# Kernel tuning notes

Measured on AMD Instinct MI355X. Metric: run time of the kernel, lower is better.

The kernel has to match this reference:

```python
import jax, jax.numpy as jnp
import numpy as np

N_NODES = 100000
N_EDGES = 1600000
D = 128


def _graph_conv(x, src, dst, norm_src, norm_dst, W, b):
    # DGL GraphConv, norm='both': out = D_dst^{-1/2} A D_src^{-1/2} x W + b
    xs = x * norm_src[:, None]                 # [N, d] scale by src (out-)degree
    agg = jax.ops.segment_sum(xs[src], dst, num_segments=N_NODES)  # SpMM
    hd = agg * norm_dst[:, None]
    return hd @ W + b


def setup_inputs() -> dict:
    key = jax.random.key(0)
    ks = jax.random.split(key, 9)
    h = jax.random.normal(ks[0], (N_NODES, D), dtype=jnp.float32)
    src = jax.random.randint(ks[1], (N_EDGES,), 0, N_NODES, dtype=jnp.int64)
    dst = jax.random.randint(ks[2], (N_EDGES,), 0, N_NODES, dtype=jnp.int64)
    s = 1.0 / np.sqrt(D)
    W0 = jax.random.uniform(ks[3], (D, D), jnp.float32, -s, s)
    b0 = jnp.zeros((D,), jnp.float32)
    W1 = jax.random.uniform(ks[4], (D, D), jnp.float32, -s, s)
    b1 = jnp.zeros((D,), jnp.float32)
    W2 = jax.random.uniform(ks[5], (D, D), jnp.float32, -s, s)
    b2 = jnp.zeros((D,), jnp.float32)
    return {"h": h, "src": src, "dst": dst, "W0": W0, "b0": b0,
            "W1": W1, "b1": b1, "W2": W2, "b2": b2}


def reference(h, src, dst, W0, b0, W1, b1, W2, b2):
    ones = jnp.ones((N_EDGES,), jnp.float32)
    deg_out = jnp.maximum(jax.ops.segment_sum(ones, src, num_segments=N_NODES), 1.0)
    deg_in = jnp.maximum(jax.ops.segment_sum(ones, dst, num_segments=N_NODES), 1.0)
    norm_src = deg_out ** -0.5
    norm_dst = deg_in ** -0.5

    x = jax.nn.relu(_graph_conv(h, src, dst, norm_src, norm_dst, W0, b0))
    x = jax.nn.relu(_graph_conv(x, src, dst, norm_src, norm_dst, W1, b1))
    x = _graph_conv(x, src, dst, norm_src, norm_dst, W2, b2)
    # dgl.mean_nodes over a single graph -> [1, out_size]
    return jnp.mean(x, axis=0, keepdims=True)
```

## Files before the change

### kernel.cpp

```cpp
#include <hip/hip_runtime.h>
#include <hip/hip_fp16.h>

#define N_NODES 100000
#define N_EDGES 1600000
#define D 128
#define SCAN_NB ((N_NODES + 1023) / 1024)
#define CHK 128
#define CHUNK_E (N_EDGES / CHK)
#define QTR_N 25000
#define QTR_U (QTR_N / 4)
#define PP_STRIDE (N_NODES / 4)
#define NSH8 8
#define SH8 (N_NODES / NSH8)
#define SH8_U (SH8 / 4)

typedef _Float16 f16x4 __attribute__((ext_vector_type(4)));
typedef _Float16 f16x8 __attribute__((ext_vector_type(8)));
typedef float f32x4 __attribute__((ext_vector_type(4)));
typedef float f32x2 __attribute__((ext_vector_type(2)));

__global__ __launch_bounds__(256) void
k_hist(const int* __restrict__ src, const int* __restrict__ dst,
       unsigned int* __restrict__ pp) {
    __shared__ unsigned int h[QTR_U];
    int b = blockIdx.x;
    int arr = b >> 9, q = (b >> 7) & 3, c = b & (CHK - 1);
    const int* a = arr ? dst : src;
    int lo = q * QTR_N;
    for (int i = threadIdx.x; i < QTR_U; i += 256) h[i] = 0;
    __syncthreads();
    int e0 = c * CHUNK_E;
    for (int i = e0 + threadIdx.x; i < e0 + CHUNK_E; i += 256) {
        int v = a[i] - lo;
        if ((unsigned)v < QTR_N)
            atomicAdd(&h[v >> 2], 1u << ((v & 3) * 8));
    }
    __syncthreads();
    unsigned int* po = pp + ((size_t)(arr * CHK + c)) * PP_STRIDE + q * QTR_U;
    for (int i = threadIdx.x; i < QTR_U; i += 256) po[i] = h[i];
}

__global__ void k_merge(unsigned int* __restrict__ pp,
                        int* __restrict__ cnt_src, int* __restrict__ cnt_dst) {
    int g = blockIdx.x * blockDim.x + threadIdx.x;
    if (g >= 2 * PP_STRIDE) return;
    int arr = g / PP_STRIDE, u = g % PP_STRIDE;
    unsigned int* p = pp + ((size_t)arr * CHK) * PP_STRIDE + u;
    int s0 = 0, s1 = 0, s2 = 0, s3 = 0;
#pragma unroll 8
    for (int c = 0; c < CHK; c++) {
        unsigned int v = p[(size_t)c * PP_STRIDE];
        p[(size_t)c * PP_STRIDE] =
            (unsigned)s0 | ((unsigned)s1 << 8) | ((unsigned)s2 << 16) | ((unsigned)s3 << 24);
        s0 += v & 255; s1 += (v >> 8) & 255; s2 += (v >> 16) & 255; s3 += (v >> 24) & 255;
    }
    int* cnt = arr ? cnt_dst : cnt_src;
    cnt[4 * u + 0] = s0; cnt[4 * u + 1] = s1; cnt[4 * u + 2] = s2; cnt[4 * u + 3] = s3;
}

__global__ __launch_bounds__(1024) void
k_scan1(const int* __restrict__ cnt_dst, const int* __restrict__ cnt_src,
        int* __restrict__ rpD, int* __restrict__ rpS,
        int* __restrict__ bsD, int* __restrict__ bsS) {
    __shared__ int s[1024];
    int arr = blockIdx.x / SCAN_NB, bb = blockIdx.x % SCAN_NB;
    const int* cnt = arr ? cnt_src : cnt_dst;
    int* rp1 = (arr ? rpS : rpD) + 1;
    int* bs = arr ? bsS : bsD;
    int tid = threadIdx.x;
    int i = bb * 1024 + tid;
    int v = (i < N_NODES) ? cnt[i] : 0;
    s[tid] = v;
    __syncthreads();
    for (int d = 1; d < 1024; d <<= 1) {
        int t = (tid >= d) ? s[tid - d] : 0;
        __syncthreads();
        s[tid] += t;
        __syncthreads();
    }
    if (i < N_NODES) rp1[i] = s[tid];
    if (tid == 1023) bs[bb] = s[1023];
}

__global__ void k_scan2(int* __restrict__ bsD, int* __restrict__ bsS) {
    __shared__ int s[128];
    int* bs = blockIdx.x ? bsS : bsD;
    int tid = threadIdx.x;
    int v = (tid < SCAN_NB) ? bs[tid] : 0;
    s[tid] = v;
    __syncthreads();
    for (int d = 1; d < 128; d <<= 1) {
        int t = (tid >= d) ? s[tid - d] : 0;
        __syncthreads();
        s[tid] += t;
        __syncthreads();
    }
    if (tid < SCAN_NB) bs[tid] = s[tid] - v;
}

__global__ void k_scan3norm(int* __restrict__ rpD, int* __restrict__ rpS,
                            const int* __restrict__ bsD, const int* __restrict__ bsS,
                            const int* __restrict__ cnt_src, const int* __restrict__ cnt_dst,
                            float* __restrict__ ns, float* __restrict__ nd,
                            float* __restrict__ colsum) {
    int i = blockIdx.x * blockDim.x + threadIdx.x;
    if (i >= N_NODES) return;
    rpD[1 + i] += bsD[i >> 10];
    rpS[1 + i] += bsS[i >> 10];
    if (i == 0) { rpD[0] = 0; rpS[0] = 0; }
    if (i < 128) colsum[i] = 0.0f;
    ns[i] = rsqrtf((float)max(cnt_src[i], 1));
    nd[i] = rsqrtf((float)max(cnt_dst[i], 1));
}

__global__ __launch_bounds__(256) void
k_scatter_both(const int* __restrict__ src, const int* __restrict__ dst,
               const int* __restrict__ rpD, const int* __restrict__ rpS,
               const unsigned int* __restrict__ pp, const float* __restrict__ nd,
               int* __restrict__ csr_src, float* __restrict__ csrv) {
    __shared__ unsigned int cur[SH8_U];
    int which = blockIdx.x >> 10;
    int b = blockIdx.x & 1023;
    int sh = b & 7, c = b >> 3;
    int lo = sh * SH8;
    for (int i = threadIdx.x; i < SH8_U; i += 256) cur[i] = 0;
    __syncthreads();
    int e0 = c * CHUNK_E;
    if (which == 0) {
        const unsigned int* pre = pp + ((size_t)(CHK + c)) * PP_STRIDE;
        for (int i = e0 + threadIdx.x; i < e0 + CHUNK_E; i += 256) {
            int dfull = dst[i];
            int d = dfull - lo;
            if ((unsigned)d < SH8) {
                int sft = (d & 3) * 8;
                int rank = (atomicAdd(&cur[d >> 2], 1u << sft) >> sft) & 255;
                int p8 = (pre[dfull >> 2] >> ((dfull & 3) * 8)) & 255;
                csr_src[rpD[dfull] + p8 + rank] = src[i];
            }
        }
    } else {
        const unsigned int* pre = pp + (size_t)c * PP_STRIDE;
        for (int i = e0 + threadIdx.x; i < e0 + CHUNK_E; i += 256) {
            int sfull = src[i];
            int s = sfull - lo;
            if ((unsigned)s < SH8) {
                int sft = (s & 3) * 8;
                int rank = (atomicAdd(&cur[s >> 2], 1u << sft) >> sft) & 255;
                int p8 = (pre[sfull >> 2] >> ((sfull & 3) * 8)) & 255;
                csrv[rpS[sfull] + p8 + rank] = nd[dst[i]];
            }
        }
    }
}

__global__ void k_wsum(const int* __restrict__ rpS, const float* __restrict__ csrv,
                       const float* __restrict__ ns, float* __restrict__ wsum) {
    int gid = blockIdx.x * blockDim.x + threadIdx.x;
    int wv = gid >> 6, lane = gid & 63;
    int n = wv * 16 + (lane & 15);
    int off = lane >> 4;
    float s = 0.0f;
    int beg = 0, end = 0;
    if (n < N_NODES) { beg = rpS[n]; end = rpS[n + 1]; }
    for (int j = beg + off; j < end; j += 4) s += csrv[j];
    s += __shfl_xor(s, 16, 64);
    s += __shfl_xor(s, 32, 64);
    if (n < N_NODES && lane < 16) wsum[n] = s * ns[n];
}

__global__ void k_prep(const float* __restrict__ W0, const float* __restrict__ W1,
                       __half* __restrict__ Wt, const float* __restrict__ x,
                       const float* __restrict__ ns, unsigned int* __restrict__ out) {
    if (blockIdx.x < 128) {
        int i = blockIdx.x * 256 + threadIdx.x;
        int l = i >> 14, r = i & (D * D - 1);
        int n = r >> 7, k = r & 127;
        const float* W = l ? W1 : W0;
        Wt[i] = __float2half(W[k * D + n]);
        return;
    }
    int i = (blockIdx.x - 128) * 256 + threadIdx.x;
    if (i >= N_NODES * (D / 4)) return;
    int n = i >> 5;
    float4 v = ((const float4*)x)[i];
    float s = ns[n];
    int u = __builtin_amdgcn_cvt_pk_fp8_f32(v.x * s, v.y * s, 0, false);
    u = __builtin_amdgcn_cvt_pk_fp8_f32(v.z * s, v.w * s, u, true);
    out[i] = (unsigned int)u;
}

__global__ __launch_bounds__(256) void
k_spmm(const unsigned char* __restrict__ x8, const int* __restrict__ row_ptr,
       const int* __restrict__ csr_src, __half* __restrict__ agg) {
    int wave = (blockIdx.x * blockDim.x + threadIdx.x) >> 6;
    int lane = threadIdx.x & 63;
    int hf = lane >> 5, l32 = lane & 31;
    if (wave >= N_NODES) return;
    int beg = row_ptr[wave], end = row_ptr[wave + 1];
    float a0 = 0.f, a1 = 0.f, a2 = 0.f, a3 = 0.f;
    int j = beg;
    for (; j + 7 < end; j += 8) {
#pragma unroll
        for (int p = 0; p < 4; p++) {
            int s0 = csr_src[j + 2 * p];
            int s1 = csr_src[j + 2 * p + 1];
            int s = hf ? s1 : s0;
            unsigned int u = *(const unsigned int*)(x8 + (size_t)s * D + 4 * l32);
            f32x2 lo = __builtin_amdgcn_cvt_pk_f32_fp8(u, false);
            f32x2 hi = __builtin_amdgcn_cvt_pk_f32_fp8(u, true);
            a0 += lo[0]; a1 += lo[1]; a2 += hi[0]; a3 += hi[1];
        }
    }
    for (; j + 1 < end; j += 2) {
        int s0 = csr_src[j], s1 = csr_src[j + 1];
        int s = hf ? s1 : s0;
        unsigned int u = *(const unsigned int*)(x8 + (size_t)s * D + 4 * l32);
        f32x2 lo = __builtin_amdgcn_cvt_pk_f32_fp8(u, false);
        f32x2 hi = __builtin_amdgcn_cvt_pk_f32_fp8(u, true);
        a0 += lo[0]; a1 += lo[1]; a2 += hi[0]; a3 += hi[1];
    }
    if (j < end && hf == 0) {
        int s = csr_src[j];
        unsigned int u = *(const unsigned int*)(x8 + (size_t)s * D + 4 * l32);
        f32x2 lo = __builtin_amdgcn_cvt_pk_f32_fp8(u, false);
        f32x2 hi = __builtin_amdgcn_cvt_pk_f32_fp8(u, true);
        a0 += lo[0]; a1 += lo[1]; a2 += hi[0]; a3 += hi[1];
    }
    a0 += __shfl_xor(a0, 32, 64);
    a1 += __shfl_xor(a1, 32, 64);
    a2 += __shfl_xor(a2, 32, 64);
    a3 += __shfl_xor(a3, 32, 64);
    if (hf == 0) {
        f16x4 o;
        o[0] = (_Float16)a0; o[1] = (_Float16)a1; o[2] = (_Float16)a2; o[3] = (_Float16)a3;
        ((f16x4*)(agg + (size_t)wave * D))[l32] = o;
    }
}

__global__ __launch_bounds__(256) void
k_gemm_mfma(const __half* __restrict__ A, const __half* __restrict__ Wt,
            const float* __restrict__ b, const float* __restrict__ nd,
            const float* __restrict__ ns, unsigned char* __restrict__ out) {
    int w = threadIdx.x >> 6, lane = threadIdx.x & 63;
    int m = lane & 15, q = lane >> 4;
    int row0 = blockIdx.x * 128 + w * 32;

    f16x8 zf;
#pragma unroll
    for (int j = 0; j < 8; j++) zf[j] = (_Float16)0;
    f16x8 af[2][4];
#pragma unroll
    for (int g = 0; g < 2; g++) {
        int arow = row0 + g * 16 + m;
        const f16x8* pa = (const f16x8*)(A + (size_t)arow * D);
        bool aok = arow < N_NODES;
#pragma unroll
        for (int ks = 0; ks < 4; ks++) af[g][ks] = aok ? pa[ks * 4 + q] : zf;
    }

    const f16x8* pb = (const f16x8*)Wt;
    f32x4 acc[2][8];
#pragma unroll
    for (int g = 0; g < 2; g++)
#pragma unroll
        for (int nt = 0; nt < 8; nt++) acc[g][nt] = (f32x4){0.f, 0.f, 0.f, 0.f};

#pragma unroll
    for (int ks = 0; ks < 4; ks++) {
#pragma unroll
        for (int nt = 0; nt < 8; nt++) {
            f16x8 bf = pb[((nt * 16 + m) << 4) + (ks << 2) + q];
            acc[0][nt] = __builtin_amdgcn_mfma_f32_16x16x32_f16(af[0][ks], bf, acc[0][nt], 0, 0, 0);
            acc[1][nt] = __builtin_amdgcn_mfma_f32_16x16x32_f16(af[1][ks], bf, acc[1][nt], 0, 0, 0);
        }
    }

#pragma unroll
    for (int g = 0; g < 2; g++) {
        int er = row0 + g * 16 + q * 4;
        float sd[4], ss[4];
#pragma unroll
        for (int r = 0; r < 4; r++) {
            int n = er + r;
            bool ok = n < N_NODES;
            sd[r] = ok ? nd[n] : 0.0f;
            ss[r] = ok ? ns[n] : 0.0f;
        }
#pragma unroll
        for (int nt = 0; nt < 8; nt++) {
            int col = nt * 16 + m;
            float bc = b[col];
#pragma unroll
            for (int r = 0; r < 4; r++) {
                int n = er + r;
                if (n < N_NODES) {
                    float v = fmaxf(sd[r] * acc[g][nt][r] + bc, 0.0f) * ss[r];
                    int pk = __builtin_amdgcn_cvt_pk_fp8_f32(v, v, 0, false);
                    out[(size_t)n * D + col] = (unsigned char)(pk & 0xff);
                }
            }
        }
    }
}

__global__ __launch_bounds__(256) void
k_gemm_red(const __half* __restrict__ A, const __half* __restrict__ Wt,
           const float* __restrict__ b, const float* __restrict__ nd,
           const float* __restrict__ wsum, float* __restrict__ colsum) {
    __shared__ float red[128];
    int tid = threadIdx.x;
    if (tid < 128) red[tid] = 0.0f;
    __syncthreads();

    int w = tid >> 6, lane = tid & 63;
    int m = lane & 15, q = lane >> 4;
    int row0 = blockIdx.x * 128 + w * 32;

    f16x8 zf;
#pragma unroll
    for (int j = 0; j < 8; j++) zf[j] = (_Float16)0;
    f16x8 af[2][4];
#pragma unroll
    for (int g = 0; g < 2; g++) {
        int arow = row0 + g * 16 + m;
        const f16x8* pa = (const f16x8*)(A + (size_t)arow * D);
        bool aok = arow < N_NODES;
#pragma unroll
        for (int ks = 0; ks < 4; ks++) af[g][ks] = aok ? pa[ks * 4 + q] : zf;
    }

    const f16x8* pb = (const f16x8*)Wt;
    f32x4 acc[2][8];
#pragma unroll
    for (int g = 0; g < 2; g++)
#pragma unroll
        for (int nt = 0; nt < 8; nt++) acc[g][nt] = (f32x4){0.f, 0.f, 0.f, 0.f};

#pragma unroll
    for (int ks = 0; ks < 4; ks++) {
#pragma unroll
        for (int nt = 0; nt < 8; nt++) {
            f16x8 bf = pb[((nt * 16 + m) << 4) + (ks << 2) + q];
            acc[0][nt] = __builtin_amdgcn_mfma_f32_16x16x32_f16(af[0][ks], bf, acc[0][nt], 0, 0, 0);
            acc[1][nt] = __builtin_amdgcn_mfma_f32_16x16x32_f16(af[1][ks], bf, acc[1][nt], 0, 0, 0);
        }
    }

    float sd[2][4], sw[2][4];
#pragma unroll
    for (int g = 0; g < 2; g++) {
        int er = row0 + g * 16 + q * 4;
#pragma unroll
        for (int r = 0; r < 4; r++) {
            int n = er + r;
            bool ok = n < N_NODES;
            sd[g][r] = ok ? nd[n] : 0.0f;
            sw[g][r] = ok ? wsum[n] : 0.0f;
        }
    }
#pragma unroll
    for (int nt = 0; nt < 8; nt++) {
        int col = nt * 16 + m;
        float bc = b[col];
        float pc = 0.0f;
#pragma unroll
        for (int g = 0; g < 2; g++)
#pragma unroll
            for (int r = 0; r < 4; r++)
                pc += sw[g][r] * fmaxf(sd[g][r] * acc[g][nt][r] + bc, 0.0f);
        atomicAdd(&red[col], pc);
    }
    __syncthreads();
    if (tid < 128) unsafeAtomicAdd(&colsum[tid], red[tid]);
}

__global__ void k_final(const float* __restrict__ colsum, const float* __restrict__ W,
                        const float* __restrict__ b, float* __restrict__ out) {
    __shared__ float m[128];
    int j = threadIdx.x;
    m[j] = colsum[j] * (1.0f / N_NODES);
    __syncthreads();
    float acc = b[j];
    for (int k = 0; k < 128; k++)
        acc = fmaf(m[k], W[(size_t)k * D + j], acc);
    out[j] = acc;
}

extern "C" void kernel_launch(void* const* d_in, const int* in_sizes, int n_in,
                              void* d_out, int out_size, void* d_ws, size_t ws_size,
                              hipStream_t stream) {
    const float* h   = (const float*)d_in[0];
    const int*   src = (const int*)d_in[1];
    const int*   dst = (const int*)d_in[2];
    const float* W0  = (const float*)d_in[3];
    const float* b0  = (const float*)d_in[4];
    const float* W1  = (const float*)d_in[5];
    const float* b1  = (const float*)d_in[6];
    const float* W2  = (const float*)d_in[7];
    const float* b2  = (const float*)d_in[8];
    float* out = (float*)d_out;

    float*         ns      = (float*)d_ws;
    float*         nd      = ns + N_NODES;
    float*         wsum    = nd + N_NODES;
    float*         colsum  = wsum + N_NODES;
    int*           rpD     = (int*)(colsum + 128);
    int*           rpS     = rpD + N_NODES + 1;
    int*           cnt_src = rpS + N_NODES + 1;
    int*           cnt_dst = cnt_src + N_NODES;
    int*           bsD     = cnt_dst + N_NODES;
    int*           bsS     = bsD + 128;
    __half*        Wt16    = (__half*)(bsS + 128);
    int*           csr_src = (int*)(Wt16 + 2 * D * D);
    float*         csrv    = (float*)(csr_src + N_EDGES);
    unsigned int*  pp      = (unsigned int*)(csrv + N_EDGES);
    unsigned char* x8      = (unsigned char*)pp;
    __half*        agg16   = (__half*)(pp + 2 * (size_t)CHK * PP_STRIDE);

    k_hist<<<2 * 4 * CHK, 256, 0, stream>>>(src, dst, pp);
    k_merge<<<(2 * PP_STRIDE + 255) / 256, 256, 0, stream>>>(pp, cnt_src, cnt_dst);
    k_scan1<<<2 * SCAN_NB, 1024, 0, stream>>>(cnt_dst, cnt_src, rpD, rpS, bsD, bsS);
    k_scan2<<<2, 128, 0, stream>>>(bsD, bsS);
    k_scan3norm<<<(N_NODES + 255) / 256, 256, 0, stream>>>(rpD, rpS, bsD, bsS,
                                                           cnt_src, cnt_dst, ns, nd, colsum);
    k_scatter_both<<<2 * NSH8 * CHK, 256, 0, stream>>>(src, dst, rpD, rpS, pp, nd,
                                                       csr_src, csrv);
    k_wsum<<<(N_NODES * 4 + 255) / 256, 256, 0, stream>>>(rpS, csrv, ns, wsum);

    k_prep<<<128 + (N_NODES * (D / 4) + 255) / 256, 256, 0, stream>>>(
        W0, W1, Wt16, h, ns, (unsigned int*)x8);

    k_spmm<<<(N_NODES + 3) / 4, 256, 0, stream>>>(x8, rpD, csr_src, agg16);
    k_gemm_mfma<<<(N_NODES + 127) / 128, 256, 0, stream>>>(agg16, Wt16, b0, nd, ns, x8);
    k_spmm<<<(N_NODES + 3) / 4, 256, 0, stream>>>(x8, rpD, csr_src, agg16);
    k_gemm_red<<<(N_NODES + 127) / 128, 256, 0, stream>>>(agg16, Wt16 + (size_t)D * D,
                                                          b1, nd, wsum, colsum);
    k_final<<<1, 128, 0, stream>>>(colsum, W2, b2, out);
}
```

Before: 448.7 us.

## Replace source-CSR construction with shared-memory atomic accumulation of per-source weights

Drops building the src-sorted CSR (scan, scatter of nd values, and per-row reduction) used only to compute wsum. Instead it accumulates nd[dst] per source node directly with LDS float atomics over 16 node ranges × 32 edge groups, then merges the partials. The dst scatter also moves from 8 to 4 node shards per chunk, which doubles the LDS counter array. The trade-off is that every edge array is now re-read once per range block, and float atomic summation order is no longer deterministic.

```diff
diff --git a/kernel.cpp b/kernel.cpp
--- a/kernel.cpp
+++ b/kernel.cpp
@@ -10,9 +10,13 @@
 #define QTR_N 25000
 #define QTR_U (QTR_N / 4)
 #define PP_STRIDE (N_NODES / 4)
-#define NSH8 8
-#define SH8 (N_NODES / NSH8)
-#define SH8_U (SH8 / 4)
+#define NSH4 4
+#define SH4 (N_NODES / NSH4)
+#define SH4_U (SH4 / 4)
+#define WR 16
+#define WRN (N_NODES / WR)
+#define WG 32
+#define WGE (N_EDGES / WG)
 
 typedef _Float16 f16x4 __attribute__((ext_vector_type(4)));
 typedef _Float16 f16x8 __attribute__((ext_vector_type(8)));
@@ -47,28 +51,32 @@
     int arr = g / PP_STRIDE, u = g % PP_STRIDE;
     unsigned int* p = pp + ((size_t)arr * CHK) * PP_STRIDE + u;
     int s0 = 0, s1 = 0, s2 = 0, s3 = 0;
+    if (arr == 0) {
 #pragma unroll 8
-    for (int c = 0; c < CHK; c++) {
-        unsigned int v = p[(size_t)c * PP_STRIDE];
-        p[(size_t)c * PP_STRIDE] =
-            (unsigned)s0 | ((unsigned)s1 << 8) | ((unsigned)s2 << 16) | ((unsigned)s3 << 24);
-        s0 += v & 255; s1 += (v >> 8) & 255; s2 += (v >> 16) & 255; s3 += (v >> 24) & 255;
-    }
-    int* cnt = arr ? cnt_dst : cnt_src;
-    cnt[4 * u + 0] = s0; cnt[4 * u + 1] = s1; cnt[4 * u + 2] = s2; cnt[4 * u + 3] = s3;
+        for (int c = 0; c < CHK; c++) {
+            unsigned int v = p[(size_t)c * PP_STRIDE];
+            s0 += v & 255; s1 += (v >> 8) & 255; s2 += (v >> 16) & 255; s3 += (v >> 24) & 255;
+        }
+        cnt_src[4 * u + 0] = s0; cnt_src[4 * u + 1] = s1;
+        cnt_src[4 * u + 2] = s2; cnt_src[4 * u + 3] = s3;
+    } else {
+#pragma unroll 8
+        for (int c = 0; c < CHK; c++) {
+            unsigned int v = p[(size_t)c * PP_STRIDE];
+            p[(size_t)c * PP_STRIDE] =
+                (unsigned)s0 | ((unsigned)s1 << 8) | ((unsigned)s2 << 16) | ((unsigned)s3 << 24);
+            s0 += v & 255; s1 += (v >> 8) & 255; s2 += (v >> 16) & 255; s3 += (v >> 24) & 255;
+        }
+        cnt_dst[4 * u + 0] = s0; cnt_dst[4 * u + 1] = s1;
+        cnt_dst[4 * u + 2] = s2; cnt_dst[4 * u + 3] = s3;
+    }
 }
 
 __global__ __launch_bounds__(1024) void
-k_scan1(const int* __restrict__ cnt_dst, const int* __restrict__ cnt_src,
-        int* __restrict__ rpD, int* __restrict__ rpS,
-        int* __restrict__ bsD, int* __restrict__ bsS) {
+k_scan1(const int* __restrict__ cnt, int* __restrict__ rp1, int* __restrict__ bs) {
     __shared__ int s[1024];
-    int arr = blockIdx.x / SCAN_NB, bb = blockIdx.x % SCAN_NB;
-    const int* cnt = arr ? cnt_src : cnt_dst;
-    int* rp1 = (arr ? rpS : rpD) + 1;
-    int* bs = arr ? bsS : bsD;
     int tid = threadIdx.x;
-    int i = bb * 1024 + tid;
+    int i = blockIdx.x * 1024 + tid;
     int v = (i < N_NODES) ? cnt[i] : 0;
     s[tid] = v;
     __syncthreads();
@@ -79,12 +87,11 @@
         __syncthreads();
     }
     if (i < N_NODES) rp1[i] = s[tid];
-    if (tid == 1023) bs[bb] = s[1023];
-}
-
-__global__ void k_scan2(int* __restrict__ bsD, int* __restrict__ bsS) {
+    if (tid == 1023) bs[blockIdx.x] = s[1023];
+}
+
+__global__ void k_scan2(int* __restrict__ bs) {
     __shared__ int s[128];
-    int* bs = blockIdx.x ? bsS : bsD;
     int tid = threadIdx.x;
     int v = (tid < SCAN_NB) ? bs[tid] : 0;
     s[tid] = v;
@@ -98,74 +105,70 @@
     if (tid < SCAN_NB) bs[tid] = s[tid] - v;
 }
 
-__global__ void k_scan3norm(int* __restrict__ rpD, int* __restrict__ rpS,
-                            const int* __restrict__ bsD, const int* __restrict__ bsS,
+__global__ void k_scan3norm(int* __restrict__ rpD, const int* __restrict__ bsD,
                             const int* __restrict__ cnt_src, const int* __restrict__ cnt_dst,
                             float* __restrict__ ns, float* __restrict__ nd,
                             float* __restrict__ colsum) {
     int i = blockIdx.x * blockDim.x + threadIdx.x;
     if (i >= N_NODES) return;
     rpD[1 + i] += bsD[i >> 10];
-    rpS[1 + i] += bsS[i >> 10];
-    if (i == 0) { rpD[0] = 0; rpS[0] = 0; }
+    if (i == 0) rpD[0] = 0;
     if (i < 128) colsum[i] = 0.0f;
     ns[i] = rsqrtf((float)max(cnt_src[i], 1));
     nd[i] = rsqrtf((float)max(cnt_dst[i], 1));
 }
 
 __global__ __launch_bounds__(256) void
-k_scatter_both(const int* __restrict__ src, const int* __restrict__ dst,
-               const int* __restrict__ rpD, const int* __restrict__ rpS,
-               const unsigned int* __restrict__ pp, const float* __restrict__ nd,
-               int* __restrict__ csr_src, float* __restrict__ csrv) {
-    __shared__ unsigned int cur[SH8_U];
-    int which = blockIdx.x >> 10;
-    int b = blockIdx.x & 1023;
-    int sh = b & 7, c = b >> 3;
-    int lo = sh * SH8;
-    for (int i = threadIdx.x; i < SH8_U; i += 256) cur[i] = 0;
+k_scatter_dst(const int* __restrict__ src, const int* __restrict__ dst,
+              const int* __restrict__ rpD, const unsigned int* __restrict__ pp,
+              int* __restrict__ csr_src) {
+    __shared__ unsigned int cur[SH4_U];
+    int sh = blockIdx.x & 3, c = blockIdx.x >> 2;
+    int lo = sh * SH4;
+    const unsigned int* pre = pp + ((size_t)(CHK + c)) * PP_STRIDE;
+    for (int i = threadIdx.x; i < SH4_U; i += 256) cur[i] = 0;
     __syncthreads();
     int e0 = c * CHUNK_E;
-    if (which == 0) {
-        const unsigned int* pre = pp + ((size_t)(CHK + c)) * PP_STRIDE;
-        for (int i = e0 + threadIdx.x; i < e0 + CHUNK_E; i += 256) {
-            int dfull = dst[i];
-            int d = dfull - lo;
-            if ((unsigned)d < SH8) {
-                int sft = (d & 3) * 8;
-                int rank = (atomicAdd(&cur[d >> 2], 1u << sft) >> sft) & 255;
-                int p8 = (pre[dfull >> 2] >> ((dfull & 3) * 8)) & 255;
-                csr_src[rpD[dfull] + p8 + rank] = src[i];
-            }
-        }
-    } else {
-        const unsigned int* pre = pp + (size_t)c * PP_STRIDE;
-        for (int i = e0 + threadIdx.x; i < e0 + CHUNK_E; i += 256) {
-            int sfull = src[i];
-            int s = sfull - lo;
-            if ((unsigned)s < SH8) {
-                int sft = (s & 3) * 8;
-                int rank = (atomicAdd(&cur[s >> 2], 1u << sft) >> sft) & 255;
-                int p8 = (pre[sfull >> 2] >> ((sfull & 3) * 8)) & 255;
-                csrv[rpS[sfull] + p8 + rank] = nd[dst[i]];
-            }
-        }
-    }
-}
-
-__global__ void k_wsum(const int* __restrict__ rpS, const float* __restrict__ csrv,
-                       const float* __restrict__ ns, float* __restrict__ wsum) {
-    int gid = blockIdx.x * blockDim.x + threadIdx.x;
-    int wv = gid >> 6, lane = gid & 63;
-    int n = wv * 16 + (lane & 15);
-    int off = lane >> 4;
+    for (int i = e0 + threadIdx.x; i < e0 + CHUNK_E; i += 256) {
+        int dfull = dst[i];
+        int d = dfull - lo;
+        if ((unsigned)d < SH4) {
+            int sft = (d & 3) * 8;
+            int rank = (atomicAdd(&cur[d >> 2], 1u << sft) >> sft) & 255;
+            int p8 = (pre[dfull >> 2] >> ((dfull & 3) * 8)) & 255;
+            csr_src[rpD[dfull] + p8 + rank] = src[i];
+        }
+    }
+}
+
+__global__ __launch_bounds__(256) void
+k_wacc(const int* __restrict__ src, const int* __restrict__ dst,
+       const float* __restrict__ nd, float* __restrict__ wpart) {
+    __shared__ float acc[WRN];
+    int r = blockIdx.x & (WR - 1), g = blockIdx.x >> 4;
+    int lo = r * WRN;
+    for (int i = threadIdx.x; i < WRN; i += 256) acc[i] = 0.0f;
+    __syncthreads();
+    int e0 = g * WGE;
+    for (int i = e0 + threadIdx.x; i < e0 + WGE; i += 256) {
+        int s = src[i] - lo;
+        if ((unsigned)s < WRN) atomicAdd(&acc[s], nd[dst[i]]);
+    }
+    __syncthreads();
+    float* po = wpart + ((size_t)g * WR + r) * WRN;
+    for (int i = threadIdx.x; i < WRN; i += 256) po[i] = acc[i];
+}
+
+__global__ void k_wmerge(const float* __restrict__ wpart, const float* __restrict__ ns,
+                         float* __restrict__ wsum) {
+    int n = blockIdx.x * blockDim.x + threadIdx.x;
+    if (n >= N_NODES) return;
+    int r = n / WRN, local = n % WRN;
     float s = 0.0f;
-    int beg = 0, end = 0;
-    if (n < N_NODES) { beg = rpS[n]; end = rpS[n + 1]; }
-    for (int j = beg + off; j < end; j += 4) s += csrv[j];
-    s += __shfl_xor(s, 16, 64);
-    s += __shfl_xor(s, 32, 64);
-    if (n < N_NODES && lane < 16) wsum[n] = s * ns[n];
+#pragma unroll 8
+    for (int g = 0; g < WG; g++)
+        s += wpart[((size_t)g * WR + r) * WRN + local];
+    wsum[n] = s * ns[n];
 }
 
 __global__ void k_prep(const float* __restrict__ W0, const float* __restrict__ W1,
@@ -405,27 +408,25 @@
     float*         wsum    = nd + N_NODES;
     float*         colsum  = wsum + N_NODES;
     int*           rpD     = (int*)(colsum + 128);
-    int*           rpS     = rpD + N_NODES + 1;
-    int*           cnt_src = rpS + N_NODES + 1;
+    int*           cnt_src = rpD + N_NODES + 1;
     int*           cnt_dst = cnt_src + N_NODES;
     int*           bsD     = cnt_dst + N_NODES;
-    int*           bsS     = bsD + 128;
-    __half*        Wt16    = (__half*)(bsS + 128);
+    __half*        Wt16    = (__half*)(bsD + 128);
     int*           csr_src = (int*)(Wt16 + 2 * D * D);
-    float*         csrv    = (float*)(csr_src + N_EDGES);
-    unsigned int*  pp      = (unsigned int*)(csrv + N_EDGES);
+    float*         wpart   = (float*)(csr_src + N_EDGES);
+    unsigned int*  pp      = (unsigned int*)(wpart + (size_t)WG * WR * WRN);
     unsigned char* x8      = (unsigned char*)pp;
     __half*        agg16   = (__half*)(pp + 2 * (size_t)CHK * PP_STRIDE);
 
     k_hist<<<2 * 4 * CHK, 256, 0, stream>>>(src, dst, pp);
     k_merge<<<(2 * PP_STRIDE + 255) / 256, 256, 0, stream>>>(pp, cnt_src, cnt_dst);
-    k_scan1<<<2 * SCAN_NB, 1024, 0, stream>>>(cnt_dst, cnt_src, rpD, rpS, bsD, bsS);
-    k_scan2<<<2, 128, 0, stream>>>(bsD, bsS);
-    k_scan3norm<<<(N_NODES + 255) / 256, 256, 0, stream>>>(rpD, rpS, bsD, bsS,
-                                                           cnt_src, cnt_dst, ns, nd, colsum);
-    k_scatter_both<<<2 * NSH8 * CHK, 256, 0, stream>>>(src, dst, rpD, rpS, pp, nd,
-                                                       csr_src, csrv);
-    k_wsum<<<(N_NODES * 4 + 255) / 256, 256, 0, stream>>>(rpS, csrv, ns, wsum);
+    k_scan1<<<SCAN_NB, 1024, 0, stream>>>(cnt_dst, rpD + 1, bsD);
+    k_scan2<<<1, 128, 0, stream>>>(bsD);
+    k_scan3norm<<<(N_NODES + 255) / 256, 256, 0, stream>>>(rpD, bsD, cnt_src, cnt_dst,
+                                                           ns, nd, colsum);
+    k_scatter_dst<<<NSH4 * CHK, 256, 0, stream>>>(src, dst, rpD, pp, csr_src);
+    k_wacc<<<WG * WR, 256, 0, stream>>>(src, dst, nd, wpart);
+    k_wmerge<<<(N_NODES + 255) / 256, 256, 0, stream>>>(wpart, ns, wsum);
 
     k_prep<<<128 + (N_NODES * (D / 4) + 255) / 256, 256, 0, stream>>>(
         W0, W1, Wt16, h, ns, (unsigned int*)x8);
```

After: 525.9 us. 1.17x slower.
